# Performance work log

Hardware: AMD Instinct MI355X
Metric: run time of the kernel (lower is better)

Reference implementation:

```python
import jax, jax.numpy as jnp
import numpy as np

B, S, D = 1, 2048, 2048
H, KVH, HD = 32, 8, 64
FFN = 8192
N_EXPERTS, TOP_K = 32, 4
EPS = 1e-5
NEG = -1e9


def setup_inputs() -> dict:
    key = jax.random.key(0)
    ks = jax.random.split(key, 24)
    s = 0.02
    inp = {}
    inp['hidden_states'] = jax.random.normal(ks[0], (B, S, D), jnp.float32)
    # RoPE tables: cos/sin of shape [B, S, HD]
    inv_freq = 1.0 / (10000.0 ** (np.arange(0, HD, 2, dtype=np.float32) / HD))
    t = np.arange(S, dtype=np.float32)
    freqs = np.outer(t, inv_freq)                      # [S, HD/2]
    emb = np.concatenate([freqs, freqs], axis=-1)      # [S, HD]
    inp['cos'] = jnp.asarray(np.cos(emb))[None].repeat(B, axis=0)
    inp['sin'] = jnp.asarray(np.sin(emb))[None].repeat(B, axis=0)
    # additive causal mask [B, 1, S, S]
    causal = jnp.where(jnp.tril(jnp.ones((S, S), bool)), 0.0, NEG).astype(jnp.float32)
    inp['attention_mask'] = jnp.broadcast_to(causal[None, None], (B, 1, S, S))
    # attention params
    inp['wq'] = jax.random.normal(ks[1], (H * HD, D), jnp.float32) * s
    inp['bq'] = jnp.zeros((H * HD,), jnp.float32)
    inp['wk'] = jax.random.normal(ks[2], (KVH * HD, D), jnp.float32) * s
    inp['bk'] = jnp.zeros((KVH * HD,), jnp.float32)
    inp['wv'] = jax.random.normal(ks[3], (KVH * HD, D), jnp.float32) * s
    inp['bv'] = jnp.zeros((KVH * HD,), jnp.float32)
    inp['wo'] = jax.random.normal(ks[4], (D, H * HD), jnp.float32) * s
    inp['bo'] = jnp.zeros((D,), jnp.float32)
    # norms
    inp['ln1_w'] = jnp.ones((D,), jnp.float32)
    inp['ln2_w'] = jnp.ones((D,), jnp.float32)
    # MoE gate + shared expert MLP
    inp['gate_w'] = jax.random.normal(ks[5], (N_EXPERTS, D), jnp.float32) * s
    inp['gate_b'] = jnp.zeros((N_EXPERTS,), jnp.float32)
    inp['w1'] = jax.random.normal(ks[6], (FFN, D), jnp.float32) * s
    inp['b1'] = jnp.zeros((FFN,), jnp.float32)
    inp['w2'] = jax.random.normal(ks[7], (D, FFN), jnp.float32) * s
    inp['b2'] = jnp.zeros((D,), jnp.float32)
    inp['w3'] = jax.random.normal(ks[8], (FFN, D), jnp.float32) * s
    inp['b3'] = jnp.zeros((FFN,), jnp.float32)
    return inp


def _rms_norm(x, w, eps=EPS):
    x32 = x.astype(jnp.float32)
    var = jnp.mean(x32 * x32, axis=-1, keepdims=True)
    return (w * (x32 * jax.lax.rsqrt(var + eps))).astype(x.dtype)


def _rotate_half(x):
    x1, x2 = jnp.split(x, 2, axis=-1)
    return jnp.concatenate([-x2, x1], axis=-1)


def _decoder_layer(hidden_states, cos, sin, attention_mask,
                   wq, bq, wk, bk, wv, bv, wo, bo, ln1_w, ln2_w,
                   gate_w, gate_b, w1, b1, w2, b2, w3, b3):
    residual = hidden_states
    x = _rms_norm(hidden_states, ln1_w)

    # projections -> [B, heads, S, HD]
    q = (x @ wq.T + bq).reshape(B, S, H, HD).transpose(0, 2, 1, 3)
    k = (x @ wk.T + bk).reshape(B, S, KVH, HD).transpose(0, 2, 1, 3)
    v = (x @ wv.T + bv).reshape(B, S, KVH, HD).transpose(0, 2, 1, 3)

    # RoPE (cos/sin unsqueezed on head dim)
    c, s_ = cos[:, None], sin[:, None]
    q = q * c + _rotate_half(q) * s_
    k = k * c + _rotate_half(k) * s_

    # GQA: repeat kv heads
    n_rep = H // KVH
    k = jnp.repeat(k, n_rep, axis=1)
    v = jnp.repeat(v, n_rep, axis=1)

    scaling = HD ** -0.5
    scores = jnp.einsum('bhqd,bhkd->bhqk', q, k) * scaling + attention_mask
    probs = jax.nn.softmax(scores.astype(jnp.float32), axis=-1).astype(q.dtype)
    attn = jnp.einsum('bhqk,bhkd->bhqd', probs, v)
    attn = attn.transpose(0, 2, 1, 3).reshape(B, S, H * HD)
    attn = attn @ wo.T + bo

    hidden_states = residual + attn
    residual = hidden_states
    x = _rms_norm(hidden_states, ln2_w)

    # MoE block (as written in source: router computed, but ALL tokens go
    # through one shared expert MLP; routing weights unused in output)
    flat = x.reshape(-1, D)
    router_logits = flat @ gate_w.T + gate_b                     # [B*S, E]
    rw = jax.nn.softmax(router_logits.astype(jnp.float32), axis=-1)
    rw_top, sel = jax.lax.top_k(rw, TOP_K)                       # computed, unused
    del rw_top, sel

    h1 = flat @ w1.T + b1
    h3 = flat @ w3.T + b3
    mlp = (jax.nn.silu(h1) * h3) @ w2.T + b2
    hidden_states = residual + mlp.reshape(B, S, D)
    return hidden_states


def reference(hidden_states, cos, sin, attention_mask,
              wq, bq, wk, bk, wv, bv, wo, bo, ln1_w, ln2_w,
              gate_w, gate_b, w1, b1, w2, b2, w3, b3):
    return _decoder_layer(hidden_states, cos, sin, attention_mask,
                          wq, bq, wk, bk, wv, bv, wo, bo, ln1_w, ln2_w,
                          gate_w, gate_b, w1, b1, w2, b2, w3, b3)
```

## Files before the change

kernel.cpp:

```cpp
#include <hip/hip_runtime.h>

#define S_LEN 2048
#define DMODEL 2048
#define NH 32
#define NKV 8
#define HD 64
#define FFN_DIM 8192

typedef __attribute__((ext_vector_type(4))) float f32x4;
typedef __attribute__((ext_vector_type(16))) float f32x16;
typedef __attribute__((ext_vector_type(8))) short bf16x8;

#define MFMA(a, b, c) __builtin_amdgcn_mfma_f32_16x16x32_bf16(a, b, c, 0, 0, 0)
#define MFMA32(a, b, c) __builtin_amdgcn_mfma_f32_32x32x16_bf16(a, b, c, 0, 0, 0)

__device__ __forceinline__ ushort f2bf(float f) {
  unsigned u = __float_as_uint(f);
  unsigned r = (u + 0x7fffu + ((u >> 16) & 1u)) >> 16;
  return (ushort)r;
}
__device__ __forceinline__ float bf2f(ushort s) {
  return __uint_as_float(((unsigned)s) << 16);
}
__device__ __forceinline__ unsigned cvtpk(float a, float b) {
  unsigned r;
  asm("v_cvt_pk_bf16_f32 %0, %1, %2" : "=v"(r) : "v"(a), "v"(b));
  return r;
}

__device__ __forceinline__ void gload16(const void* g, void* l) {
  __builtin_amdgcn_global_load_lds(
      (const __attribute__((address_space(1))) void*)g,
      (__attribute__((address_space(3))) void*)l, 16, 0, 0);
}

__global__ __launch_bounds__(256) void cvt_k(const float* __restrict__ in,
                                             ushort* __restrict__ out) {
  int i = blockIdx.x * 256 + threadIdx.x;
  f32x4 a = ((const f32x4*)in)[i * 2];
  f32x4 b = ((const f32x4*)in)[i * 2 + 1];
  bf16x8 r;
#pragma unroll
  for (int j = 0; j < 4; j++) r[j] = (short)f2bf(a[j]);
#pragma unroll
  for (int j = 0; j < 4; j++) r[4 + j] = (short)f2bf(b[j]);
  ((bf16x8*)out)[i] = r;
}

__global__ __launch_bounds__(256) void cvt_qkv_k(const float* __restrict__ wq,
                                                 const float* __restrict__ wk,
                                                 const float* __restrict__ wv,
                                                 ushort* __restrict__ dst) {
  int row = blockIdx.x;
  const float* src;
  if (row < 2048) src = wq + (size_t)row * DMODEL;
  else if (row < 2560) src = wk + (size_t)(row - 2048) * DMODEL;
  else src = wv + (size_t)(row - 2560) * DMODEL;
  int i = threadIdx.x * 8;
  f32x4 a = *(const f32x4*)(src + i);
  f32x4 b = *(const f32x4*)(src + i + 4);
  bf16x8 r;
#pragma unroll
  for (int j = 0; j < 4; j++) r[j] = (short)f2bf(a[j]);
#pragma unroll
  for (int j = 0; j < 4; j++) r[4 + j] = (short)f2bf(b[j]);
  *(bf16x8*)(dst + (size_t)row * DMODEL + i) = r;
}

__global__ __launch_bounds__(256) void bias3_k(const float* __restrict__ a,
                                               const float* __restrict__ b,
                                               const float* __restrict__ c,
                                               float* __restrict__ out) {
  int i = blockIdx.x * 256 + threadIdx.x;
  float v;
  if (i < 2048) v = a[i];
  else if (i < 2560) v = b[i - 2048];
  else v = c[i - 2560];
  out[i] = v;
}

__global__ __launch_bounds__(256) void rmsnorm_k(const float* __restrict__ in,
                                                 const float* __restrict__ w,
                                                 ushort* __restrict__ out) {
  const int row = blockIdx.x;
  const int tid = threadIdx.x;
  const float* x = in + (size_t)row * DMODEL;
  f32x4 v0 = *(const f32x4*)(x + tid * 8);
  f32x4 v1 = *(const f32x4*)(x + tid * 8 + 4);
  float ss = v0[0] * v0[0] + v0[1] * v0[1] + v0[2] * v0[2] + v0[3] * v0[3] +
             v1[0] * v1[0] + v1[1] * v1[1] + v1[2] * v1[2] + v1[3] * v1[3];
#pragma unroll
  for (int off = 32; off; off >>= 1) ss += __shfl_xor(ss, off, 64);
  __shared__ float red[4];
  if ((tid & 63) == 0) red[tid >> 6] = ss;
  __syncthreads();
  float tot = red[0] + red[1] + red[2] + red[3];
  float inv = rsqrtf(tot * (1.f / DMODEL) + 1e-5f);
#pragma unroll
  for (int i = 0; i < 8; i++) {
    int c = tid * 8 + i;
    float val = (i < 4) ? v0[i] : v1[i - 4];
    out[(size_t)row * DMODEL + c] = f2bf(w[c] * val * inv);
  }
}

__global__ __launch_bounds__(256) void rope_k(ushort* __restrict__ qkv,
                                              const float* __restrict__ cs,
                                              const float* __restrict__ sn) {
  int idx = blockIdx.x * 256 + threadIdx.x;
  int d = idx & 31;
  int t = idx >> 5;
  int head = t % (NH + NKV);
  int s = t / (NH + NKV);
  int col = (head < NH) ? head * HD : DMODEL + (head - NH) * HD;
  ushort* p = qkv + (size_t)s * 3072 + col;
  float lo = bf2f(p[d]), hi = bf2f(p[d + 32]);
  float c = cs[s * HD + d], si = sn[s * HD + d];
  p[d] = f2bf(lo * c - hi * si);
  p[d + 32] = f2bf(hi * c + lo * si);
}

enum { EPI_BF16 = 0, EPI_RESID = 1, EPI_SILU = 2, EPI_MUL = 3, EPI_PART = 4 };

__device__ __forceinline__ void quad(const bf16x8* Arr, const bf16x8* BR,
                                     f32x4 (*accr)[4], int qn) {
#pragma unroll
  for (int i = 0; i < 4; i++)
#pragma unroll
    for (int j = 0; j < 2; j++)
#pragma unroll
      for (int ks = 0; ks < 2; ks++)
        accr[i][qn * 2 + j] =
            MFMA(Arr[2 * i + ks], BR[2 * j + ks], accr[i][qn * 2 + j]);
}

template <int EPI>
__global__ __launch_bounds__(512, 2) void gemm256(
    const ushort* __restrict__ A, int lda, const ushort* __restrict__ B,
    int ldb, const float* __restrict__ bias, const float* __restrict__ resid,
    ushort* __restrict__ outb, float* __restrict__ outf, int ldc, int K,
    int kspan, long long opart) {
  __shared__ __align__(16) ushort lds[65536];
  const int tid = threadIdx.x;
  const int l = tid & 63, w = tid >> 6;
  const int g = l >> 4, r16 = l & 15;
  const int wm = w >> 2, wn = w & 3;

  int nwg = gridDim.x * gridDim.y;
  int bid = blockIdx.y * gridDim.x + blockIdx.x;
  bid = (bid & 7) * (nwg >> 3) + (bid >> 3);
  const int m0 = (bid % gridDim.x) * 256;
  const int n0 = (bid / gridDim.x) * 256;
  const int z = blockIdx.z;

  const ushort* Ag = A + (size_t)z * kspan + (size_t)m0 * lda;
  const ushort* Bg = B + (size_t)z * kspan + (size_t)n0 * ldb;
  ushort* outbz = outb;
  if (EPI == EPI_PART) outbz = outb + (size_t)z * opart;

  const int NT = K >> 6;

  const int stgRow = w * 8 + (l >> 3);
  const int stgCol = ((l & 7) ^ (l >> 3)) * 8;

  const int xa = (r16 & 7) << 4;
  const int c0 = ((g * 16) ^ xa) >> 1;
  const int c1 = c0 ^ 32;
  const int slotA = wm ? 3 : 1;
  const int slotB = (wn >> 1) ? 2 : 0;
  const ushort* pA0 = lds + slotA * 8192 + r16 * 64 + c0;
  const ushort* pA1 = lds + slotA * 8192 + r16 * 64 + c1;
  const ushort* pB0 = lds + slotB * 8192 + ((wn & 1) * 64 + r16) * 64 + c0;
  const ushort* pB1 = lds + slotB * 8192 + ((wn & 1) * 64 + r16) * 64 + c1;

  f32x4 acc[8][4];
#pragma unroll
  for (int i = 0; i < 8; i++)
#pragma unroll
    for (int j = 0; j < 4; j++) acc[i][j] = (f32x4){0, 0, 0, 0};

  auto stageA = [&](int slot, int tile, int hf) {
    ushort* dst = lds + ((tile & 1) * 32768 + slot * 8192 + w * 512);
    const ushort* src =
        Ag + (size_t)(hf * 128 + stgRow) * lda + tile * 64 + stgCol;
    gload16(src, dst);
    gload16(src + (size_t)64 * lda, dst + 4096);
  };
  auto stageB = [&](int slot, int tile, int hf) {
    ushort* dst = lds + ((tile & 1) * 32768 + slot * 8192 + w * 512);
    const ushort* src =
        Bg + (size_t)(hf * 128 + stgRow) * ldb + tile * 64 + stgCol;
    gload16(src, dst);
    gload16(src + (size_t)64 * ldb, dst + 4096);
  };

  stageB(0, 0, 0);
  stageA(1, 0, 0);
  stageB(2, 0, 1);
  stageA(3, 0, 1);
  stageB(0, 1, 0);
  stageA(1, 1, 0);
  asm volatile("s_waitcnt vmcnt(4)" ::: "memory");
  __builtin_amdgcn_s_barrier();

  bf16x8 Ar[8], Br0[4], Br1[4];

  for (int t = 0; t < NT; ++t) {
    const int bo = (t & 1) * 32768;
#pragma unroll
    for (int i = 0; i < 4; i++) {
      Ar[2 * i] = *(const bf16x8*)(pA0 + bo + i * 1024);
      Ar[2 * i + 1] = *(const bf16x8*)(pA1 + bo + i * 1024);
    }
#pragma unroll
    for (int j = 0; j < 2; j++) {
      Br0[2 * j] = *(const bf16x8*)(pB0 + bo + j * 1024);
      Br0[2 * j + 1] = *(const bf16x8*)(pB1 + bo + j * 1024);
    }
    if (t + 1 < NT) stageB(2, t + 1, 1);
    __builtin_amdgcn_s_barrier();
    __builtin_amdgcn_s_setprio(1);
    quad(Ar, Br0, &acc[0], 0);
    __builtin_amdgcn_s_setprio(0);
    __builtin_amdgcn_s_barrier();
#pragma unroll
    for (int j = 0; j < 2; j++) {
      Br1[2 * j] = *(const bf16x8*)(pB0 + bo + (j + 2) * 1024);
      Br1[2 * j + 1] = *(const bf16x8*)(pB1 + bo + (j + 2) * 1024);
    }
    if (t + 1 < NT) stageA(3, t + 1, 1);
    __builtin_amdgcn_s_barrier();
    __builtin_amdgcn_s_setprio(1);
    quad(Ar, Br1, &acc[0], 1);
    __builtin_amdgcn_s_setprio(0);
    __builtin_amdgcn_s_barrier();
#pragma unroll
    for (int i = 0; i < 4; i++) {
      Ar[2 * i] = *(const bf16x8*)(pA0 + bo + (i + 4) * 1024);
      Ar[2 * i + 1] = *(const bf16x8*)(pA1 + bo + (i + 4) * 1024);
    }
    if (t + 2 < NT) stageB(0, t + 2, 0);
    __builtin_amdgcn_s_barrier();
    __builtin_amdgcn_s_setprio(1);
    quad(Ar, Br1, &acc[4], 1);
    __builtin_amdgcn_s_setprio(0);
    __builtin_amdgcn_s_barrier();
    if (t + 2 < NT) stageA(1, t + 2, 0);
    __builtin_amdgcn_s_barrier();
    __builtin_amdgcn_s_setprio(1);
    quad(Ar, Br0, &acc[4], 0);
    __builtin_amdgcn_s_setprio(0);
    if (t + 2 < NT) {
      asm volatile("s_waitcnt vmcnt(4)" ::: "memory");
    } else {
      asm volatile("s_waitcnt vmcnt(0)" ::: "memory");
    }
    __builtin_amdgcn_s_barrier();
  }

#pragma unroll
  for (int mf = 0; mf < 8; mf++) {
#pragma unroll
    for (int nf = 0; nf < 4; nf++) {
      const int n = n0 + wn * 64 + nf * 16 + r16;
      float bia = (EPI == EPI_PART) ? 0.f : bias[n];
#pragma unroll
      for (int reg = 0; reg < 4; reg++) {
        const int m = m0 + wm * 128 + mf * 16 + g * 4 + reg;
        float v = acc[mf][nf][reg] + bia;
        if constexpr (EPI == EPI_BF16) {
          outbz[(size_t)m * ldc + n] = f2bf(v);
        } else if constexpr (EPI == EPI_RESID) {
          outf[(size_t)m * ldc + n] = v + resid[(size_t)m * ldc + n];
        } else if constexpr (EPI == EPI_SILU) {
          float sv = v / (1.f + __expf(-v));
          outbz[(size_t)m * ldc + n] = f2bf(sv);
        } else if constexpr (EPI == EPI_MUL) {
          float hv = bf2f(outbz[(size_t)m * ldc + n]);
          outbz[(size_t)m * ldc + n] = f2bf(v * hv);
        } else {
          outbz[(size_t)m * ldc + n] = f2bf(v);
        }
      }
    }
  }
}

template <int MODE>
__global__ __launch_bounds__(256) void reduce2_k(
    const ushort* __restrict__ part, long long pstride, int nz,
    const float* __restrict__ bias, int ncol, const float* __restrict__ resid,
    float* __restrict__ outf, ushort* __restrict__ outb) {
  long long i = (long long)(blockIdx.x * 256 + threadIdx.x) * 8;
  int col = (int)(i % ncol);
  float s[8];
#pragma unroll
  for (int j = 0; j < 8; j++) s[j] = bias[col + j];
  for (int zz = 0; zz < nz; zz++) {
    bf16x8 v = *(const bf16x8*)(part + zz * pstride + i);
#pragma unroll
    for (int j = 0; j < 8; j++) s[j] += bf2f((ushort)v[j]);
  }
  if constexpr (MODE == 1) {
#pragma unroll
    for (int j = 0; j < 8; j++) outf[i + j] = s[j] + resid[i + j];
  } else {
    bf16x8 r;
#pragma unroll
    for (int j = 0; j < 8; j++) r[j] = (short)f2bf(s[j]);
    *(bf16x8*)(outb + i) = r;
  }
}

__global__ __launch_bounds__(256, 3) void flash2_k(const ushort* __restrict__ qkv,
                                                   ushort* __restrict__ att) {
  const int bid = blockIdx.x;
  const int head = (bid >> 4) & 31;
  const int rmap = bid & 15;
  const int qb = (bid & 256) ? (15 - rmap) : rmap;
  const int kvh = head >> 2;
  const int tid = threadIdx.x;
  const int w = tid >> 6, l = tid & 63;
  const int h = l >> 5, q31 = l & 31;
  const int qw = qb * 128 + w * 32;
  const int qrow = qw + q31;

  __shared__ __align__(16) ushort lds[2][8192];

  bf16x8 qreg[4];
  {
    const ushort* qp = qkv + (size_t)qrow * 3072 + head * HD;
#pragma unroll
    for (int s = 0; s < 4; s++)
      qreg[s] = *(const bf16x8*)(qp + s * 16 + h * 8);
  }

  f32x16 oacc[2];
#pragma unroll
  for (int i = 0; i < 16; i++) { oacc[0][i] = 0.f; oacc[1][i] = 0.f; }
  float mreg = -1e30f, lsum = 0.f;

  const int nt = 2 * qb + 2;

  const int skv = tid >> 2;
  const int sch = (tid & 3) * 2;
  const int vkv = tid & 63;
  const int vd0 = (tid >> 6) * 16;

  const ushort* kg_base = qkv + DMODEL + kvh * HD;

  bf16x8 krA, krB, vrA, vrB;
  auto loadTile = [&](int jb) {
    const ushort* kg = kg_base + (size_t)jb * 64 * 3072;
    krA = *(const bf16x8*)(kg + (size_t)skv * 3072 + sch * 8);
    krB = *(const bf16x8*)(kg + (size_t)skv * 3072 + sch * 8 + 8);
    const ushort* vg = kg + 512;
    vrA = *(const bf16x8*)(vg + (size_t)vkv * 3072 + vd0);
    vrB = *(const bf16x8*)(vg + (size_t)vkv * 3072 + vd0 + 8);
  };
  auto writeTile = [&](int b) {
    ushort* kb = lds[b];
    *(bf16x8*)(kb + skv * 64 + ((sch ^ (skv & 7)) * 8)) = krA;
    *(bf16x8*)(kb + skv * 64 + (((sch + 1) ^ (skv & 7)) * 8)) = krB;
    ushort* vb = lds[b] + 4096;
#pragma unroll
    for (int i = 0; i < 8; i++) {
      int d = vd0 + i;
      vb[d * 64 + (((vkv >> 3) ^ (d & 7)) * 8) + (vkv & 7)] = (ushort)vrA[i];
    }
#pragma unroll
    for (int i = 0; i < 8; i++) {
      int d = vd0 + 8 + i;
      vb[d * 64 + (((vkv >> 3) ^ (d & 7)) * 8) + (vkv & 7)] = (ushort)vrB[i];
    }
  };

  loadTile(0);
  for (int jb = 0; jb < nt; ++jb) {
    const int b = jb & 1;
    writeTile(b);
    __syncthreads();
    if (jb + 1 < nt) loadTile(jb + 1);

    if (jb * 64 <= qw + 31) {
      const ushort* Kb = lds[b];
      const ushort* Vb = lds[b] + 4096;

      f32x16 sacc[2];
#pragma unroll
      for (int i = 0; i < 16; i++) { sacc[0][i] = 0.f; sacc[1][i] = 0.f; }
#pragma unroll
      for (int c = 0; c < 2; c++) {
        const int kvr = c * 32 + q31;
        const ushort* kp = Kb + kvr * 64;
        const int kx = kvr & 7;
#pragma unroll
        for (int s = 0; s < 4; s++) {
          bf16x8 kf = *(const bf16x8*)(kp + ((2 * s + h) ^ kx) * 8);
          sacc[c] = MFMA32(kf, qreg[s], sacc[c]);
        }
      }

      const bool diag = (jb * 64 + 63 > qw);
      if (diag) {
#pragma unroll
        for (int c = 0; c < 2; c++)
#pragma unroll
          for (int rg = 0; rg < 16; rg++) {
            int kvg = jb * 64 + c * 32 + (rg & 3) + 8 * (rg >> 2) + 4 * h;
            if (kvg > qrow) sacc[c][rg] = -1e30f;
          }
      }
      float tmax = sacc[0][0];
#pragma unroll
      for (int rg = 1; rg < 16; rg++) tmax = fmaxf(tmax, sacc[0][rg]);
#pragma unroll
      for (int rg = 0; rg < 16; rg++) tmax = fmaxf(tmax, sacc[1][rg]);
      tmax = fmaxf(tmax, __shfl_xor(tmax, 32));
      const float mn = fmaxf(mreg, tmax);
      const float resc = __expf((mreg - mn) * 0.125f);
      mreg = mn;
      float rsum = 0.f;
#pragma unroll
      for (int c = 0; c < 2; c++)
#pragma unroll
        for (int rg = 0; rg < 16; rg++) {
          float pv = __expf((sacc[c][rg] - mn) * 0.125f);
          sacc[c][rg] = pv;
          rsum += pv;
        }
      rsum += __shfl_xor(rsum, 32);
      lsum = lsum * resc + rsum;
      oacc[0] *= resc;
      oacc[1] *= resc;

      unsigned pw_[2][4][2];
#pragma unroll
      for (int c = 0; c < 2; c++)
#pragma unroll
        for (int rr = 0; rr < 4; rr++) {
          pw_[c][rr][0] = cvtpk(sacc[c][4 * rr + 0], sacc[c][4 * rr + 1]);
          pw_[c][rr][1] = cvtpk(sacc[c][4 * rr + 2], sacc[c][4 * rr + 3]);
        }

#pragma unroll
      for (int s = 0; s < 4; s++) {
        const int c = s >> 1, base = (s & 1) * 2;
        unsigned k0 = h ? pw_[c][base + 1][0] : pw_[c][base][0];
        unsigned k1 = h ? pw_[c][base + 1][1] : pw_[c][base][1];
        unsigned s0 = h ? pw_[c][base][0] : pw_[c][base + 1][0];
        unsigned s1 = h ? pw_[c][base][1] : pw_[c][base + 1][1];
        unsigned t0 = __shfl_xor(s0, 32);
        unsigned t1 = __shfl_xor(s1, 32);
        union { unsigned u[4]; bf16x8 v; } pf;
        pf.u[0] = h ? t0 : k0;
        pf.u[1] = h ? t1 : k1;
        pf.u[2] = h ? k0 : t0;
        pf.u[3] = h ? k1 : t1;
#pragma unroll
        for (int dt = 0; dt < 2; dt++) {
          const int d = dt * 32 + q31;
          bf16x8 vf =
              *(const bf16x8*)(Vb + d * 64 + ((2 * s + h) ^ (d & 7)) * 8);
          oacc[dt] = MFMA32(vf, pf.v, oacc[dt]);
        }
      }
    }
  }

  const float inv = 1.f / lsum;
  ushort* op = att + (size_t)qrow * DMODEL + head * HD;
#pragma unroll
  for (int dt = 0; dt < 2; dt++)
#pragma unroll
    for (int rr = 0; rr < 4; rr++) {
      const int d0 = dt * 32 + 8 * rr + 4 * h;
      unsigned lo = cvtpk(oacc[dt][4 * rr + 0] * inv, oacc[dt][4 * rr + 1] * inv);
      unsigned hi = cvtpk(oacc[dt][4 * rr + 2] * inv, oacc[dt][4 * rr + 3] * inv);
      uint2 v2;
      v2.x = lo;
      v2.y = hi;
      *(uint2*)(op + d0) = v2;
    }
}

extern "C" void kernel_launch(void* const* d_in, const int* in_sizes, int n_in,
                              void* d_out, int out_size, void* d_ws,
                              size_t ws_size, hipStream_t stream) {
  (void)in_sizes; (void)n_in; (void)out_size; (void)ws_size;
  const float* hidden = (const float*)d_in[0];
  const float* cosb = (const float*)d_in[1];
  const float* sinb = (const float*)d_in[2];
  const float* wq = (const float*)d_in[4];
  const float* bq = (const float*)d_in[5];
  const float* wk = (const float*)d_in[6];
  const float* bk = (const float*)d_in[7];
  const float* wv = (const float*)d_in[8];
  const float* bv = (const float*)d_in[9];
  const float* wo = (const float*)d_in[10];
  const float* bo = (const float*)d_in[11];
  const float* ln1 = (const float*)d_in[12];
  const float* ln2 = (const float*)d_in[13];
  const float* w1 = (const float*)d_in[16];
  const float* b1 = (const float*)d_in[17];
  const float* w2 = (const float*)d_in[18];
  const float* b2 = (const float*)d_in[19];
  const float* w3 = (const float*)d_in[20];
  const float* b3 = (const float*)d_in[21];
  float* out = (float*)d_out;

  char* ws = (char*)d_ws;
  ushort* x1 = (ushort*)ws;   ws += (size_t)S_LEN * DMODEL * 2;
  ushort* qkv = (ushort*)ws;  ws += (size_t)S_LEN * 3072 * 2;
  ushort* att = (ushort*)ws;  ws += (size_t)S_LEN * DMODEL * 2;
  ushort* x2 = (ushort*)ws;   ws += (size_t)S_LEN * DMODEL * 2;
  ushort* hbuf = (ushort*)ws; ws += (size_t)S_LEN * FFN_DIM * 2;
  ushort* wbuf = (ushort*)ws; ws += (size_t)FFN_DIM * DMODEL * 2;
  float* bqkv = (float*)ws;   ws += 3072 * 4;

  ushort* partQ = att;
  ushort* partO = x2;
  ushort* partW = x1;

  rmsnorm_k<<<S_LEN, 256, 0, stream>>>(hidden, ln1, x1);

  cvt_qkv_k<<<3072, 256, 0, stream>>>(wq, wk, wv, wbuf);
  bias3_k<<<12, 256, 0, stream>>>(bq, bk, bv, bqkv);

  gemm256<EPI_PART><<<dim3(8, 12, 2), 512, 0, stream>>>(
      x1, DMODEL, wbuf, DMODEL, nullptr, nullptr, partQ, nullptr, 3072, 1024,
      1024, (long long)S_LEN * 3072);
  reduce2_k<0><<<(S_LEN * 3072) / 2048, 256, 0, stream>>>(
      partQ, (long long)S_LEN * 3072, 2, bqkv, 3072, nullptr, nullptr, qkv);

  rope_k<<<(S_LEN * (NH + NKV) * 32) / 256, 256, 0, stream>>>(qkv, cosb, sinb);

  flash2_k<<<512, 256, 0, stream>>>(qkv, att);

  cvt_k<<<(2048 * 2048) / 2048, 256, 0, stream>>>(wo, wbuf);
  gemm256<EPI_PART><<<dim3(8, 8, 4), 512, 0, stream>>>(
      att, DMODEL, wbuf, DMODEL, nullptr, nullptr, partO, nullptr, DMODEL, 512,
      512, (long long)S_LEN * DMODEL);
  reduce2_k<1><<<(S_LEN * DMODEL) / 2048, 256, 0, stream>>>(
      partO, (long long)S_LEN * DMODEL, 4, bo, DMODEL, hidden, out, nullptr);

  rmsnorm_k<<<S_LEN, 256, 0, stream>>>(out, ln2, x2);

  cvt_k<<<(FFN_DIM * 2048) / 2048, 256, 0, stream>>>(w1, wbuf);
  gemm256<EPI_SILU><<<dim3(8, 32), 512, 0, stream>>>(
      x2, DMODEL, wbuf, DMODEL, b1, nullptr, hbuf, nullptr, FFN_DIM, DMODEL, 0,
      0);

  cvt_k<<<(FFN_DIM * 2048) / 2048, 256, 0, stream>>>(w3, wbuf);
  gemm256<EPI_MUL><<<dim3(8, 32), 512, 0, stream>>>(
      x2, DMODEL, wbuf, DMODEL, b3, nullptr, hbuf, nullptr, FFN_DIM, DMODEL, 0,
      0);

  cvt_k<<<(DMODEL * FFN_DIM) / 2048, 256, 0, stream>>>(w2, wbuf);
  gemm256<EPI_PART><<<dim3(8, 8, 4), 512, 0, stream>>>(
      hbuf, FFN_DIM, wbuf, FFN_DIM, nullptr, nullptr, partW, nullptr, DMODEL,
      DMODEL, DMODEL, (long long)S_LEN * DMODEL);
  reduce2_k<1><<<(S_LEN * DMODEL) / 2048, 256, 0, stream>>>(
      partW, (long long)S_LEN * DMODEL, 4, b2, DMODEL, out, out, nullptr);
}
```

Measured before the change: 425.3 us.

## Replace 256-tile pipelined GEMM with simple 128-tile GEMM and fuse W1/W3 gate GEMMs

Swaps the double-buffered, barrier-staged 256x256 GEMM for a single-buffered 128x128 GEMM with a plain load-sync-compute loop. It also interleaves the w1 and w3 rows into one converted weight buffer, so a single GEMM produces h1 and h3 side by side and applies silu(h1)*h3 in the epilogue. This removes one GEMM pass over x2, one weight-conversion launch and the read-modify-write of hbuf. The cost is losing the software pipelining and larger-tile reuse of the old kernel, so global-memory latency is no longer hidden behind MFMA work, and the weight buffer doubles in size.

```diff
diff --git a/kernel.cpp b/kernel.cpp
--- a/kernel.cpp
+++ b/kernel.cpp
@@ -56,6 +56,25 @@
   if (row < 2048) src = wq + (size_t)row * DMODEL;
   else if (row < 2560) src = wk + (size_t)(row - 2048) * DMODEL;
   else src = wv + (size_t)(row - 2560) * DMODEL;
+  int i = threadIdx.x * 8;
+  f32x4 a = *(const f32x4*)(src + i);
+  f32x4 b = *(const f32x4*)(src + i + 4);
+  bf16x8 r;
+#pragma unroll
+  for (int j = 0; j < 4; j++) r[j] = (short)f2bf(a[j]);
+#pragma unroll
+  for (int j = 0; j < 4; j++) r[4 + j] = (short)f2bf(b[j]);
+  *(bf16x8*)(dst + (size_t)row * DMODEL + i) = r;
+}
+
+__global__ __launch_bounds__(256) void cvt_w13_k(const float* __restrict__ w1,
+                                                 const float* __restrict__ w3,
+                                                 ushort* __restrict__ dst) {
+  int row = blockIdx.x;
+  int nb = row >> 7, i5 = row & 127;
+  int grp = i5 >> 4, e = i5 & 15;
+  int srow = nb * 64 + (grp >> 1) * 16 + e;
+  const float* src = ((grp & 1) ? w3 : w1) + (size_t)srow * DMODEL;
   int i = threadIdx.x * 8;
   f32x4 a = *(const f32x4*)(src + i);
   f32x4 b = *(const f32x4*)(src + i + 4);
@@ -120,169 +139,107 @@
   p[d + 32] = f2bf(hi * c + lo * si);
 }
 
-enum { EPI_BF16 = 0, EPI_RESID = 1, EPI_SILU = 2, EPI_MUL = 3, EPI_PART = 4 };
-
-__device__ __forceinline__ void quad(const bf16x8* Arr, const bf16x8* BR,
-                                     f32x4 (*accr)[4], int qn) {
-#pragma unroll
-  for (int i = 0; i < 4; i++)
-#pragma unroll
-    for (int j = 0; j < 2; j++)
-#pragma unroll
-      for (int ks = 0; ks < 2; ks++)
-        accr[i][qn * 2 + j] =
-            MFMA(Arr[2 * i + ks], BR[2 * j + ks], accr[i][qn * 2 + j]);
-}
+enum { EPI_PART = 0, EPI_SILU2 = 1 };
 
 template <int EPI>
-__global__ __launch_bounds__(512, 2) void gemm256(
+__global__ __launch_bounds__(256) void gemm128(
     const ushort* __restrict__ A, int lda, const ushort* __restrict__ B,
-    int ldb, const float* __restrict__ bias, const float* __restrict__ resid,
-    ushort* __restrict__ outb, float* __restrict__ outf, int ldc, int K,
-    int kspan, long long opart) {
-  __shared__ __align__(16) ushort lds[65536];
+    int ldb, const float* __restrict__ b1v, const float* __restrict__ b3v,
+    ushort* __restrict__ outb, int ldc, int K, int kspan, long long opart) {
+  __shared__ __align__(16) ushort lds[16384];
   const int tid = threadIdx.x;
   const int l = tid & 63, w = tid >> 6;
   const int g = l >> 4, r16 = l & 15;
-  const int wm = w >> 2, wn = w & 3;
+  const int wm = w >> 1, wn = w & 1;
 
   int nwg = gridDim.x * gridDim.y;
   int bid = blockIdx.y * gridDim.x + blockIdx.x;
   bid = (bid & 7) * (nwg >> 3) + (bid >> 3);
-  const int m0 = (bid % gridDim.x) * 256;
-  const int n0 = (bid / gridDim.x) * 256;
+  const int m0 = (bid % gridDim.x) * 128;
+  const int n0 = (bid / gridDim.x) * 128;
   const int z = blockIdx.z;
 
   const ushort* Ag = A + (size_t)z * kspan + (size_t)m0 * lda;
   const ushort* Bg = B + (size_t)z * kspan + (size_t)n0 * ldb;
-  ushort* outbz = outb;
-  if (EPI == EPI_PART) outbz = outb + (size_t)z * opart;
+  ushort* outbz = outb + (size_t)z * opart;
 
   const int NT = K >> 6;
 
   const int stgRow = w * 8 + (l >> 3);
   const int stgCol = ((l & 7) ^ (l >> 3)) * 8;
-
   const int xa = (r16 & 7) << 4;
   const int c0 = ((g * 16) ^ xa) >> 1;
   const int c1 = c0 ^ 32;
-  const int slotA = wm ? 3 : 1;
-  const int slotB = (wn >> 1) ? 2 : 0;
-  const ushort* pA0 = lds + slotA * 8192 + r16 * 64 + c0;
-  const ushort* pA1 = lds + slotA * 8192 + r16 * 64 + c1;
-  const ushort* pB0 = lds + slotB * 8192 + ((wn & 1) * 64 + r16) * 64 + c0;
-  const ushort* pB1 = lds + slotB * 8192 + ((wn & 1) * 64 + r16) * 64 + c1;
-
-  f32x4 acc[8][4];
-#pragma unroll
-  for (int i = 0; i < 8; i++)
+  const ushort* pA0 = lds + (wm * 64 + r16) * 64 + c0;
+  const ushort* pA1 = lds + (wm * 64 + r16) * 64 + c1;
+  const ushort* pB0 = lds + 8192 + (wn * 64 + r16) * 64 + c0;
+  const ushort* pB1 = lds + 8192 + (wn * 64 + r16) * 64 + c1;
+
+  f32x4 acc[4][4];
+#pragma unroll
+  for (int i = 0; i < 4; i++)
 #pragma unroll
     for (int j = 0; j < 4; j++) acc[i][j] = (f32x4){0, 0, 0, 0};
 
-  auto stageA = [&](int slot, int tile, int hf) {
-    ushort* dst = lds + ((tile & 1) * 32768 + slot * 8192 + w * 512);
-    const ushort* src =
-        Ag + (size_t)(hf * 128 + stgRow) * lda + tile * 64 + stgCol;
-    gload16(src, dst);
-    gload16(src + (size_t)64 * lda, dst + 4096);
-  };
-  auto stageB = [&](int slot, int tile, int hf) {
-    ushort* dst = lds + ((tile & 1) * 32768 + slot * 8192 + w * 512);
-    const ushort* src =
-        Bg + (size_t)(hf * 128 + stgRow) * ldb + tile * 64 + stgCol;
-    gload16(src, dst);
-    gload16(src + (size_t)64 * ldb, dst + 4096);
-  };
-
-  stageB(0, 0, 0);
-  stageA(1, 0, 0);
-  stageB(2, 0, 1);
-  stageA(3, 0, 1);
-  stageB(0, 1, 0);
-  stageA(1, 1, 0);
-  asm volatile("s_waitcnt vmcnt(4)" ::: "memory");
-  __builtin_amdgcn_s_barrier();
-
-  bf16x8 Ar[8], Br0[4], Br1[4];
-
   for (int t = 0; t < NT; ++t) {
-    const int bo = (t & 1) * 32768;
-#pragma unroll
-    for (int i = 0; i < 4; i++) {
-      Ar[2 * i] = *(const bf16x8*)(pA0 + bo + i * 1024);
-      Ar[2 * i + 1] = *(const bf16x8*)(pA1 + bo + i * 1024);
-    }
-#pragma unroll
-    for (int j = 0; j < 2; j++) {
-      Br0[2 * j] = *(const bf16x8*)(pB0 + bo + j * 1024);
-      Br0[2 * j + 1] = *(const bf16x8*)(pB1 + bo + j * 1024);
-    }
-    if (t + 1 < NT) stageB(2, t + 1, 1);
-    __builtin_amdgcn_s_barrier();
-    __builtin_amdgcn_s_setprio(1);
-    quad(Ar, Br0, &acc[0], 0);
-    __builtin_amdgcn_s_setprio(0);
-    __builtin_amdgcn_s_barrier();
-#pragma unroll
-    for (int j = 0; j < 2; j++) {
-      Br1[2 * j] = *(const bf16x8*)(pB0 + bo + (j + 2) * 1024);
-      Br1[2 * j + 1] = *(const bf16x8*)(pB1 + bo + (j + 2) * 1024);
-    }
-    if (t + 1 < NT) stageA(3, t + 1, 1);
-    __builtin_amdgcn_s_barrier();
-    __builtin_amdgcn_s_setprio(1);
-    quad(Ar, Br1, &acc[0], 1);
-    __builtin_amdgcn_s_setprio(0);
-    __builtin_amdgcn_s_barrier();
-#pragma unroll
-    for (int i = 0; i < 4; i++) {
-      Ar[2 * i] = *(const bf16x8*)(pA0 + bo + (i + 4) * 1024);
-      Ar[2 * i + 1] = *(const bf16x8*)(pA1 + bo + (i + 4) * 1024);
-    }
-    if (t + 2 < NT) stageB(0, t + 2, 0);
-    __builtin_amdgcn_s_barrier();
-    __builtin_amdgcn_s_setprio(1);
-    quad(Ar, Br1, &acc[4], 1);
-    __builtin_amdgcn_s_setprio(0);
-    __builtin_amdgcn_s_barrier();
-    if (t + 2 < NT) stageA(1, t + 2, 0);
-    __builtin_amdgcn_s_barrier();
-    __builtin_amdgcn_s_setprio(1);
-    quad(Ar, Br0, &acc[4], 0);
-    __builtin_amdgcn_s_setprio(0);
-    if (t + 2 < NT) {
-      asm volatile("s_waitcnt vmcnt(4)" ::: "memory");
-    } else {
-      asm volatile("s_waitcnt vmcnt(0)" ::: "memory");
-    }
-    __builtin_amdgcn_s_barrier();
-  }
-
-#pragma unroll
-  for (int mf = 0; mf < 8; mf++) {
-#pragma unroll
-    for (int nf = 0; nf < 4; nf++) {
-      const int n = n0 + wn * 64 + nf * 16 + r16;
-      float bia = (EPI == EPI_PART) ? 0.f : bias[n];
-#pragma unroll
-      for (int reg = 0; reg < 4; reg++) {
-        const int m = m0 + wm * 128 + mf * 16 + g * 4 + reg;
-        float v = acc[mf][nf][reg] + bia;
-        if constexpr (EPI == EPI_BF16) {
-          outbz[(size_t)m * ldc + n] = f2bf(v);
-        } else if constexpr (EPI == EPI_RESID) {
-          outf[(size_t)m * ldc + n] = v + resid[(size_t)m * ldc + n];
-        } else if constexpr (EPI == EPI_SILU) {
-          float sv = v / (1.f + __expf(-v));
-          outbz[(size_t)m * ldc + n] = f2bf(sv);
-        } else if constexpr (EPI == EPI_MUL) {
-          float hv = bf2f(outbz[(size_t)m * ldc + n]);
-          outbz[(size_t)m * ldc + n] = f2bf(v * hv);
-        } else {
-          outbz[(size_t)m * ldc + n] = f2bf(v);
+#pragma unroll
+    for (int p = 0; p < 4; p++) {
+      const int row = p * 32 + stgRow;
+      gload16(Ag + (size_t)row * lda + t * 64 + stgCol,
+              lds + (p * 32 + w * 8) * 64);
+      gload16(Bg + (size_t)row * ldb + t * 64 + stgCol,
+              lds + 8192 + (p * 32 + w * 8) * 64);
+    }
+    __syncthreads();
+    bf16x8 Ar[8], Br[8];
+#pragma unroll
+    for (int mt = 0; mt < 4; mt++) {
+      Ar[2 * mt] = *(const bf16x8*)(pA0 + mt * 1024);
+      Ar[2 * mt + 1] = *(const bf16x8*)(pA1 + mt * 1024);
+    }
+#pragma unroll
+    for (int nt = 0; nt < 4; nt++) {
+      Br[2 * nt] = *(const bf16x8*)(pB0 + nt * 1024);
+      Br[2 * nt + 1] = *(const bf16x8*)(pB1 + nt * 1024);
+    }
+#pragma unroll
+    for (int kk = 0; kk < 2; kk++)
+#pragma unroll
+      for (int mt = 0; mt < 4; mt++)
+#pragma unroll
+        for (int nt = 0; nt < 4; nt++)
+          acc[mt][nt] = MFMA(Ar[2 * mt + kk], Br[2 * nt + kk], acc[mt][nt]);
+    __syncthreads();
+  }
+
+  if constexpr (EPI == EPI_PART) {
+#pragma unroll
+    for (int mf = 0; mf < 4; mf++)
+#pragma unroll
+      for (int nf = 0; nf < 4; nf++) {
+        const int n = n0 + wn * 64 + nf * 16 + r16;
+#pragma unroll
+        for (int reg = 0; reg < 4; reg++) {
+          const int m = m0 + wm * 64 + mf * 16 + g * 4 + reg;
+          outbz[(size_t)m * ldc + n] = f2bf(acc[mf][nf][reg]);
         }
       }
-    }
+  } else {
+#pragma unroll
+    for (int mf = 0; mf < 4; mf++)
+#pragma unroll
+      for (int p = 0; p < 2; p++) {
+        const int col = (n0 >> 1) + wn * 32 + p * 16 + r16;
+        const float bb1 = b1v[col], bb3 = b3v[col];
+#pragma unroll
+        for (int reg = 0; reg < 4; reg++) {
+          const int m = m0 + wm * 64 + mf * 16 + g * 4 + reg;
+          float h1 = acc[mf][2 * p][reg] + bb1;
+          float h3 = acc[mf][2 * p + 1][reg] + bb3;
+          float sv = h1 / (1.f + __expf(-h1));
+          outbz[(size_t)m * ldc + col] = f2bf(sv * h3);
+        }
+      }
   }
 }
 
@@ -515,7 +472,7 @@
   ushort* att = (ushort*)ws;  ws += (size_t)S_LEN * DMODEL * 2;
   ushort* x2 = (ushort*)ws;   ws += (size_t)S_LEN * DMODEL * 2;
   ushort* hbuf = (ushort*)ws; ws += (size_t)S_LEN * FFN_DIM * 2;
-  ushort* wbuf = (ushort*)ws; ws += (size_t)FFN_DIM * DMODEL * 2;
+  ushort* wbuf = (ushort*)ws; ws += (size_t)FFN_DIM * DMODEL * 2 * 2;
   float* bqkv = (float*)ws;   ws += 3072 * 4;
 
   ushort* partQ = att;
@@ -527,9 +484,9 @@
   cvt_qkv_k<<<3072, 256, 0, stream>>>(wq, wk, wv, wbuf);
   bias3_k<<<12, 256, 0, stream>>>(bq, bk, bv, bqkv);
 
-  gemm256<EPI_PART><<<dim3(8, 12, 2), 512, 0, stream>>>(
-      x1, DMODEL, wbuf, DMODEL, nullptr, nullptr, partQ, nullptr, 3072, 1024,
-      1024, (long long)S_LEN * 3072);
+  gemm128<EPI_PART><<<dim3(16, 24, 2), 256, 0, stream>>>(
+      x1, DMODEL, wbuf, DMODEL, nullptr, nullptr, partQ, 3072, 1024, 1024,
+      (long long)S_LEN * 3072);
   reduce2_k<0><<<(S_LEN * 3072) / 2048, 256, 0, stream>>>(
       partQ, (long long)S_LEN * 3072, 2, bqkv, 3072, nullptr, nullptr, qkv);
 
@@ -538,28 +495,22 @@
   flash2_k<<<512, 256, 0, stream>>>(qkv, att);
 
   cvt_k<<<(2048 * 2048) / 2048, 256, 0, stream>>>(wo, wbuf);
-  gemm256<EPI_PART><<<dim3(8, 8, 4), 512, 0, stream>>>(
-      att, DMODEL, wbuf, DMODEL, nullptr, nullptr, partO, nullptr, DMODEL, 512,
-      512, (long long)S_LEN * DMODEL);
+  gemm128<EPI_PART><<<dim3(16, 16, 4), 256, 0, stream>>>(
+      att, DMODEL, wbuf, DMODEL, nullptr, nullptr, partO, DMODEL, 512, 512,
+      (long long)S_LEN * DMODEL);
   reduce2_k<1><<<(S_LEN * DMODEL) / 2048, 256, 0, stream>>>(
       partO, (long long)S_LEN * DMODEL, 4, bo, DMODEL, hidden, out, nullptr);
 
   rmsnorm_k<<<S_LEN, 256, 0, stream>>>(out, ln2, x2);
 
-  cvt_k<<<(FFN_DIM * 2048) / 2048, 256, 0, stream>>>(w1, wbuf);
-  gemm256<EPI_SILU><<<dim3(8, 32), 512, 0, stream>>>(
-      x2, DMODEL, wbuf, DMODEL, b1, nullptr, hbuf, nullptr, FFN_DIM, DMODEL, 0,
-      0);
-
-  cvt_k<<<(FFN_DIM * 2048) / 2048, 256, 0, stream>>>(w3, wbuf);
-  gemm256<EPI_MUL><<<dim3(8, 32), 512, 0, stream>>>(
-      x2, DMODEL, wbuf, DMODEL, b3, nullptr, hbuf, nullptr, FFN_DIM, DMODEL, 0,
-      0);
+  cvt_w13_k<<<2 * FFN_DIM, 256, 0, stream>>>(w1, w3, wbuf);
+  gemm128<EPI_SILU2><<<dim3(16, 128), 256, 0, stream>>>(
+      x2, DMODEL, wbuf, DMODEL, b1, b3, hbuf, FFN_DIM, DMODEL, 0, 0);
 
   cvt_k<<<(DMODEL * FFN_DIM) / 2048, 256, 0, stream>>>(w2, wbuf);
-  gemm256<EPI_PART><<<dim3(8, 8, 4), 512, 0, stream>>>(
-      hbuf, FFN_DIM, wbuf, FFN_DIM, nullptr, nullptr, partW, nullptr, DMODEL,
-      DMODEL, DMODEL, (long long)S_LEN * DMODEL);
+  gemm128<EPI_PART><<<dim3(16, 16, 4), 256, 0, stream>>>(
+      hbuf, FFN_DIM, wbuf, FFN_DIM, nullptr, nullptr, partW, DMODEL, 2048,
+      2048, (long long)S_LEN * DMODEL);
   reduce2_k<1><<<(S_LEN * DMODEL) / 2048, 256, 0, stream>>>(
       partW, (long long)S_LEN * DMODEL, 4, b2, DMODEL, out, out, nullptr);
 }
```

Result: slower. 459.0 us (+7.9%).
